# Optimization experiments

Hardware: AMD Instinct MI355X
Metric: run time of the kernel (lower is better)

## Reference

```python
import jax, jax.numpy as jnp
import numpy as np

EPS = 1e-8  # torch.nn.CosineSimilarity default eps


def _cosine_sim(a, b):
    # cosine similarity along channel dim (axis=1), matching torch semantics:
    # dot / (max(||a||, eps) * max(||b||, eps))
    na = jnp.maximum(jnp.sqrt(jnp.sum(a * a, axis=1)), EPS)
    nb = jnp.maximum(jnp.sqrt(jnp.sum(b * b, axis=1)), EPS)
    return jnp.sum(a * b, axis=1) / (na * nb)  # [B, T]


def setup_inputs() -> dict:
    key = jax.random.key(0)
    k1, k2, k3 = jax.random.split(key, 3)
    B, C, T, O, K = 8, 512, 4096, 512, 3
    feature = jax.random.normal(k1, (B, C, T), dtype=jnp.float32)
    embedding = jax.random.normal(k2, (B, C, T), dtype=jnp.float32)
    weight = jax.random.normal(k3, (O, C, K), dtype=jnp.float32) * 0.05
    return {"feature": feature, "embedding": embedding, "weight": weight}


def reference(feature, embedding, weight):
    B, C, T = feature.shape
    O = weight.shape[0]
    K = 3  # kernel_size is structurally 3 in this module

    # shifted embeddings with zero padding (left / right neighbors)
    emb_l = jnp.pad(embedding[:, :, :-1], ((0, 0), (0, 0), (1, 0)))
    emb_r = jnp.pad(embedding[:, :, 1:], ((0, 0), (0, 0), (0, 1)))
    sim = jnp.stack(
        [_cosine_sim(embedding, emb_l),
         _cosine_sim(embedding, embedding),
         _cosine_sim(embedding, emb_r)],
        axis=1,
    )  # [B, 3, T]

    # tile: first C rows = sim_l, next C = sim_c, last C = sim_r -> [B, 3C, T]
    att = jnp.repeat(sim, C, axis=1)

    # im2col (nn.Unfold with kernel (3,1), padding (1,0)): channel-major layout
    f_pad = jnp.pad(feature, ((0, 0), (0, 0), (1, 1)))  # [B, C, T+2]
    inp_unf = jnp.stack([f_pad[:, :, k:k + T] for k in range(K)], axis=2)
    inp_unf = inp_unf.reshape(B, C * K, T)  # row index = c*3 + k (torch unfold order)

    w_flat = weight.reshape(O, C * K)
    # out[b,o,t] = sum_i (inp_unf * att)[b,i,t] * w_flat[o,i]
    out = jnp.einsum('bit,oi->bot', inp_unf * att, w_flat)
    return out
```

## Files before the change

kernel.cpp:

```cpp
#include <hip/hip_runtime.h>
#include <hip/hip_bf16.h>
#include <stdint.h>

#define B_ 8
#define C_ 512
#define T_ 4096
#define O_ 512
#define KP_ 1728
#define EPS_ 1e-8f

#define BM 256
#define BN 128
#define FTP_ROWS 4104

#define RING_USH 12288
#define LDS_BYTES (4 * RING_USH * 2)

typedef unsigned short ushort_t;
typedef __attribute__((ext_vector_type(4))) float f32x4;
typedef __attribute__((ext_vector_type(8))) short bf16x8;

__device__ __forceinline__ ushort_t f2bf(float f) {
  union { float f; uint32_t u; } x; x.f = f;
  uint32_t u = x.u;
  uint32_t r = (u + 0x7FFFu + ((u >> 16) & 1u)) >> 16;
  return (ushort_t)r;
}

#define GLOAD16(gsrc, ldst) \
  __builtin_amdgcn_global_load_lds((const __attribute__((address_space(1))) unsigned int*)(gsrc), \
                                   (__attribute__((address_space(3))) unsigned int*)(ldst), 16, 0, 0)

__global__ void sim_reduce_kernel(const float* __restrict__ emb,
                                  float* __restrict__ nn_out,
                                  float* __restrict__ dl_out) {
  const int b = blockIdx.y;
  const int t0 = (blockIdx.x * 64 + threadIdx.x) * 4;
  const int cty = threadIdx.y;
  float nn0=0.f,nn1=0.f,nn2=0.f,nn3=0.f;
  float dl0=0.f,dl1=0.f,dl2=0.f,dl3=0.f;
  const float* base = emb + (size_t)b * C_ * T_;
  for (int c = cty * 128; c < cty * 128 + 128; ++c) {
    const float* row = base + (size_t)c * T_;
    float4 v = *(const float4*)(row + t0);
    float el = (t0 > 0) ? row[t0 - 1] : 0.f;
    nn0 += v.x*v.x; nn1 += v.y*v.y; nn2 += v.z*v.z; nn3 += v.w*v.w;
    dl0 += v.x*el;  dl1 += v.y*v.x; dl2 += v.z*v.y; dl3 += v.w*v.z;
  }
  __shared__ float red[4][64*8];
  float* myr = &red[cty][threadIdx.x * 8];
  if (cty != 0) {
    myr[0]=nn0; myr[1]=nn1; myr[2]=nn2; myr[3]=nn3;
    myr[4]=dl0; myr[5]=dl1; myr[6]=dl2; myr[7]=dl3;
  }
  __syncthreads();
  if (cty == 0) {
    for (int q = 1; q < 4; ++q) {
      float* r = &red[q][threadIdx.x * 8];
      nn0+=r[0]; nn1+=r[1]; nn2+=r[2]; nn3+=r[3];
      dl0+=r[4]; dl1+=r[5]; dl2+=r[6]; dl3+=r[7];
    }
    float* nb = nn_out + (size_t)b * T_ + t0;
    float* db = dl_out + (size_t)b * T_ + t0;
    nb[0]=nn0; nb[1]=nn1; nb[2]=nn2; nb[3]=nn3;
    db[0]=dl0; db[1]=dl1; db[2]=dl2; db[3]=dl3;
  }
}

__global__ void prep_small_kernel(const float* __restrict__ nn,
                                  const float* __restrict__ dl,
                                  float* __restrict__ sim,
                                  const float* __restrict__ w,
                                  ushort_t* __restrict__ wbf) {
  const int bid = blockIdx.x;
  if (bid < 128) {
    const int idx = bid * 256 + threadIdx.x;
    const int b = idx >> 12;
    const int t = idx & (T_ - 1);
    const float* nnb = nn + (size_t)b * T_;
    const float* dlb = dl + (size_t)b * T_;
    float nncur = nnb[t];
    float ncur = fmaxf(sqrtf(nncur), EPS_);
    float sc = nncur / (ncur * ncur);
    float sl = 0.f, sr = 0.f;
    if (t > 0) {
      float np = fmaxf(sqrtf(nnb[t - 1]), EPS_);
      sl = dlb[t] / (ncur * np);
    }
    if (t < T_ - 1) {
      float nx = fmaxf(sqrtf(nnb[t + 1]), EPS_);
      sr = dlb[t + 1] / (ncur * nx);
    }
    float* simb = sim + (size_t)b * 3 * T_;
    simb[t] = sl;
    simb[T_ + t] = sc;
    simb[2 * T_ + t] = sr;
  } else {
    const int idx = (bid - 128) * 256 + threadIdx.x;
    if (idx >= O_ * KP_) return;
    const int o = idx / KP_;
    const int p = idx - o * KP_;
    const int g = p / 576; const int r = p - g * 576;
    const int k = r / 192; const int j = r - k * 192;
    const int c_lo = (512 * g - k + 2) / 3;
    const int c_hi = (512 * g + 511 - k) / 3;
    const int c = (c_lo & ~7) + j;
    float v = (c >= c_lo && c <= c_hi) ? w[((size_t)o * C_ + c) * 3 + k] : 0.f;
    wbf[idx] = f2bf(v);
  }
}

__global__ void transpose_kernel(const float* __restrict__ feat, ushort_t* __restrict__ Ftp) {
  const int b = blockIdx.z;
  const int c0 = blockIdx.y * 64;
  const int tid = threadIdx.x;
  if (blockIdx.x == T_ / 64) {
    if (tid < 64)        Ftp[((size_t)b * FTP_ROWS + 0) * 512 + c0 + tid] = 0;
    else if (tid < 128)  Ftp[((size_t)b * FTP_ROWS + T_ + 1) * 512 + c0 + (tid - 64)] = 0;
    return;
  }
  const int t0 = blockIdx.x * 64;
  __shared__ ushort_t LT[64 * 72];
  {
    const int cl = tid >> 2;
    const int tq = (tid & 3) * 16;
    const float* src = feat + ((size_t)b * C_ + c0 + cl) * T_ + t0 + tq;
    for (int q = 0; q < 4; ++q) {
      float4 v = *(const float4*)(src + q * 4);
      const int t = tq + q * 4;
      LT[(t + 0) * 72 + cl] = f2bf(v.x);
      LT[(t + 1) * 72 + cl] = f2bf(v.y);
      LT[(t + 2) * 72 + cl] = f2bf(v.z);
      LT[(t + 3) * 72 + cl] = f2bf(v.w);
    }
  }
  __syncthreads();
  {
    const int tl = tid >> 2;
    const int cq = (tid & 3) * 16;
    ushort_t* dst = Ftp + ((size_t)b * FTP_ROWS + t0 + tl + 1) * 512 + c0 + cq;
    *(uint4*)(dst) = *(const uint4*)&LT[tl * 72 + cq];
    *(uint4*)(dst + 8) = *(const uint4*)&LT[tl * 72 + cq + 8];
  }
}

__global__ __launch_bounds__(512, 2)
void conv_gemm_kernel(const ushort_t* __restrict__ Ftp,
                      const ushort_t* __restrict__ wbf,
                      const float* __restrict__ sim,
                      float* __restrict__ out) {
  extern __shared__ ushort_t lds[];

  const int b = blockIdx.z;
  const int oBase = blockIdx.y * BM;
  const int tBase = blockIdx.x * BN;

  const int tid = threadIdx.x;
  const int lane = tid & 63;
  const int wid = tid >> 6;
  const int wm = wid >> 1;
  const int wn = wid & 1;
  const int llo = lane & 15, lhi = lane >> 4;

  const int rdsw = ((lhi ^ ((llo >> 1) & 3)) << 3);
  const int gch = ((lane & 3) ^ ((lane >> 3) & 3)) << 3;
  const int arow = wid * 32 + (lane >> 2);
  const int brow = wid * 16 + (lane >> 2);

  const ushort_t* ftpB = Ftp + (size_t)b * FTP_ROWS * 512;
  const float* simB = sim + (size_t)b * 3 * T_;

  float sv[3][4];
#pragma unroll
  for (int g = 0; g < 3; ++g)
#pragma unroll
    for (int n = 0; n < 4; ++n) {
      sv[g][n] = simB[g * T_ + tBase + wn * 64 + n * 16 + llo];
      asm volatile("" : "+v"(sv[g][n]));
    }
  asm volatile("s_waitcnt vmcnt(0)" ::: "memory");

  f32x4 cacc[4][4], oacc[4][4];
  const f32x4 vzero = {0.f, 0.f, 0.f, 0.f};
#pragma unroll
  for (int m = 0; m < 4; ++m)
#pragma unroll
    for (int n = 0; n < 4; ++n) { cacc[m][n] = vzero; oacc[m][n] = vzero; }

  auto STAGE = [&](int u) {
    const int s2 = u >> 1, h = u & 1;
    const int g = s2 / 9, r = s2 - g * 9, k = r / 3, jb = r - k * 3;
    const int c_st = ((512 * g - k + 2) / 3) & ~7;
    ushort_t* ring = lds + (u & 3) * RING_USH;
    const ushort_t* aS = wbf + (size_t)(oBase + arow) * KP_ + s2 * 64 + h * 32 + gch;
    GLOAD16(aS, ring + wid * 1024);
    GLOAD16(aS + (size_t)16 * KP_, ring + wid * 1024 + 512);
    const ushort_t* bS = ftpB + (size_t)(tBase + brow + k) * 512 + c_st + jb * 64 + h * 32 + gch;
    GLOAD16(bS, ring + 8192 + wid * 512);
  };

  auto PHASE = [&](int u, int vm) {
    if (vm == 6)      { asm volatile("s_waitcnt vmcnt(6)" ::: "memory"); }
    else if (vm == 3) { asm volatile("s_waitcnt vmcnt(3)" ::: "memory"); }
    else              { asm volatile("s_waitcnt vmcnt(0)" ::: "memory"); }
    __builtin_amdgcn_s_barrier();
    asm volatile("" ::: "memory");

    const ushort_t* Ah = lds + (u & 3) * RING_USH;
    const ushort_t* Bh = Ah + 8192;
    bf16x8 af[4], bfv[4];
#pragma unroll
    for (int m = 0; m < 4; ++m)
      af[m] = *(const bf16x8*)&Ah[(wm * 64 + m * 16 + llo) * 32 + rdsw];
#pragma unroll
    for (int n = 0; n < 4; ++n)
      bfv[n] = *(const bf16x8*)&Bh[(wn * 64 + n * 16 + llo) * 32 + rdsw];

    if (u + 3 < 54) STAGE(u + 3);

    __builtin_amdgcn_s_setprio(1);
#pragma unroll
    for (int m = 0; m < 4; ++m)
#pragma unroll
      for (int n = 0; n < 4; ++n)
        cacc[m][n] = __builtin_amdgcn_mfma_f32_16x16x32_bf16(af[m], bfv[n], cacc[m][n], 0, 0, 0);
    __builtin_amdgcn_s_setprio(0);

    asm volatile("s_waitcnt lgkmcnt(0)" ::: "memory");
    __builtin_amdgcn_sched_barrier(0);
  };

  STAGE(0); STAGE(1); STAGE(2);

#pragma unroll
  for (int s = 0; s < 27; ++s) {
    const int u0 = 2 * s, u1 = 2 * s + 1;
    PHASE(u0, u0 < 52 ? 6 : 3);
    PHASE(u1, u1 < 52 ? 6 : 0);
    if (s == 8 || s == 17 || s == 26) {
      const int g = s / 9;
#pragma unroll
      for (int n = 0; n < 4; ++n) {
        const float sc = sv[g][n];
#pragma unroll
        for (int m = 0; m < 4; ++m) {
          oacc[m][n] += sc * cacc[m][n];
          cacc[m][n] = vzero;
        }
      }
    }
  }

  float* outB = out + ((size_t)b * O_ + oBase) * T_ + tBase;
#pragma unroll
  for (int m = 0; m < 4; ++m) {
    const int r0 = wm * 64 + m * 16 + lhi * 4;
#pragma unroll
    for (int n = 0; n < 4; ++n) {
      const int cg = wn * 64 + n * 16 + llo;
#pragma unroll
      for (int r = 0; r < 4; ++r)
        outB[(size_t)(r0 + r) * T_ + cg] = oacc[m][n][r];
    }
  }
}

extern "C" void kernel_launch(void* const* d_in, const int* in_sizes, int n_in,
                              void* d_out, int out_size, void* d_ws, size_t ws_size,
                              hipStream_t stream) {
  const float* feature   = (const float*)d_in[0];
  const float* embedding = (const float*)d_in[1];
  const float* weight    = (const float*)d_in[2];
  float* out = (float*)d_out;

  float* ws  = (float*)d_ws;
  float* nn  = ws;
  float* dl  = nn + (size_t)B_ * T_;
  float* sim = dl + (size_t)B_ * T_;
  ushort_t* wbf = (ushort_t*)(sim + (size_t)3 * B_ * T_);
  ushort_t* Ftp = wbf + (size_t)O_ * KP_;

  (void)hipFuncSetAttribute((const void*)conv_gemm_kernel,
                            hipFuncAttributeMaxDynamicSharedMemorySize, LDS_BYTES);

  sim_reduce_kernel<<<dim3(T_ / 256, B_), dim3(64, 4), 0, stream>>>(embedding, nn, dl);
  prep_small_kernel<<<dim3(128 + (O_ * KP_ + 255) / 256), 256, 0, stream>>>(nn, dl, sim, weight, wbf);
  transpose_kernel<<<dim3(T_ / 64 + 1, C_ / 64, B_), 256, 0, stream>>>(feature, Ftp);
  conv_gemm_kernel<<<dim3(T_ / BN, O_ / BM, B_), 512, LDS_BYTES, stream>>>(Ftp, wbf, sim, out);
}
```

Measured before the change: 115.4 us.

## Load weight A-fragments directly from global into registers, stage only B in LDS

The GEMM kernel no longer stages weight tiles through LDS. Each wave loads its A fragments straight from global memory into double-buffered registers one step ahead, and only the feature (B) tiles go through a smaller 4-slot LDS ring, now static shared memory. This cuts LDS footprint and traffic and drops the A-side LDS reads and barrier dependence, with waitcnt values retuned for the changed number of in-flight loads. In exchange, A is read from global by both wn waves without coalescing-friendly staging, which raises global/L2 traffic and register pressure.

Result: slower. 177.3 us (+53.6%).

```diff
diff --git a/kernel.cpp b/kernel.cpp
--- a/kernel.cpp
+++ b/kernel.cpp
@@ -12,9 +12,6 @@
 #define BM 256
 #define BN 128
 #define FTP_ROWS 4104
-
-#define RING_USH 12288
-#define LDS_BYTES (4 * RING_USH * 2)
 
 typedef unsigned short ushort_t;
 typedef __attribute__((ext_vector_type(4))) float f32x4;
@@ -149,7 +146,7 @@
                       const ushort_t* __restrict__ wbf,
                       const float* __restrict__ sim,
                       float* __restrict__ out) {
-  extern __shared__ ushort_t lds[];
+  __shared__ __align__(16) ushort_t lds[4 * 4096];
 
   const int b = blockIdx.z;
   const int oBase = blockIdx.y * BM;
@@ -164,11 +161,14 @@
 
   const int rdsw = ((lhi ^ ((llo >> 1) & 3)) << 3);
   const int gch = ((lane & 3) ^ ((lane >> 3) & 3)) << 3;
-  const int arow = wid * 32 + (lane >> 2);
-  const int brow = wid * 16 + (lane >> 2);
 
   const ushort_t* ftpB = Ftp + (size_t)b * FTP_ROWS * 512;
   const float* simB = sim + (size_t)b * 3 * T_;
+
+  const ushort_t* aB0 = wbf + (size_t)(oBase + wm * 64 + llo) * KP_ + lhi * 8;
+  const ushort_t* aB[4] = {aB0, aB0 + 16 * KP_, aB0 + 32 * KP_, aB0 + 48 * KP_};
+
+  const ushort_t* bRow = ftpB + (size_t)(tBase + wid * 16 + (lane >> 2)) * 512 + gch;
 
   float sv[3][4];
 #pragma unroll
@@ -187,58 +187,60 @@
 #pragma unroll
     for (int n = 0; n < 4; ++n) { cacc[m][n] = vzero; oacc[m][n] = vzero; }
 
-  auto STAGE = [&](int u) {
-    const int s2 = u >> 1, h = u & 1;
+  auto GLOADB = [&](int v) {
+    const int s2 = v >> 1, h = v & 1;
     const int g = s2 / 9, r = s2 - g * 9, k = r / 3, jb = r - k * 3;
     const int c_st = ((512 * g - k + 2) / 3) & ~7;
-    ushort_t* ring = lds + (u & 3) * RING_USH;
-    const ushort_t* aS = wbf + (size_t)(oBase + arow) * KP_ + s2 * 64 + h * 32 + gch;
-    GLOAD16(aS, ring + wid * 1024);
-    GLOAD16(aS + (size_t)16 * KP_, ring + wid * 1024 + 512);
-    const ushort_t* bS = ftpB + (size_t)(tBase + brow + k) * 512 + c_st + jb * 64 + h * 32 + gch;
-    GLOAD16(bS, ring + 8192 + wid * 512);
+    GLOAD16(bRow + k * 512 + c_st + jb * 64 + h * 32, lds + (v & 3) * 4096 + wid * 512);
   };
 
-  auto PHASE = [&](int u, int vm) {
-    if (vm == 6)      { asm volatile("s_waitcnt vmcnt(6)" ::: "memory"); }
-    else if (vm == 3) { asm volatile("s_waitcnt vmcnt(3)" ::: "memory"); }
-    else              { asm volatile("s_waitcnt vmcnt(0)" ::: "memory"); }
+  bf16x8 af[2][4];
+
+  GLOADB(0); GLOADB(1); GLOADB(2);
+  __builtin_amdgcn_sched_barrier(0);
+#pragma unroll
+  for (int m = 0; m < 4; ++m)
+    af[0][m] = *(const bf16x8*)(aB[m]);
+  __builtin_amdgcn_sched_barrier(0);
+
+#pragma unroll
+  for (int u = 0; u < 54; ++u) {
+    if (u == 0)       { asm volatile("s_waitcnt vmcnt(6)"  ::: "memory"); }
+    else if (u == 1)  { asm volatile("s_waitcnt vmcnt(10)" ::: "memory"); }
+    else if (u == 52) { asm volatile("s_waitcnt vmcnt(13)" ::: "memory"); }
+    else if (u == 53) { asm volatile("s_waitcnt vmcnt(12)" ::: "memory"); }
+    else              { asm volatile("s_waitcnt vmcnt(14)" ::: "memory"); }
+    __builtin_amdgcn_sched_barrier(0);
     __builtin_amdgcn_s_barrier();
-    asm volatile("" ::: "memory");
-
-    const ushort_t* Ah = lds + (u & 3) * RING_USH;
-    const ushort_t* Bh = Ah + 8192;
-    bf16x8 af[4], bfv[4];
+    __builtin_amdgcn_sched_barrier(0);
+
+    if (u + 3 < 54) GLOADB(u + 3);
+    __builtin_amdgcn_sched_barrier(0);
+
+    if (u + 1 < 54) {
+#pragma unroll
+      for (int m = 0; m < 4; ++m)
+        af[(u + 1) & 1][m] = *(const bf16x8*)(aB[m] + (u + 1) * 32);
+    }
+    __builtin_amdgcn_sched_barrier(0);
+
+    const ushort_t* Bs = lds + (u & 3) * 4096;
+    bf16x8 bfv[4];
+#pragma unroll
+    for (int n = 0; n < 4; ++n)
+      bfv[n] = *(const bf16x8*)&Bs[(wn * 64 + n * 16 + llo) * 32 + rdsw];
+
+    __builtin_amdgcn_s_setprio(1);
 #pragma unroll
     for (int m = 0; m < 4; ++m)
-      af[m] = *(const bf16x8*)&Ah[(wm * 64 + m * 16 + llo) * 32 + rdsw];
-#pragma unroll
-    for (int n = 0; n < 4; ++n)
-      bfv[n] = *(const bf16x8*)&Bh[(wn * 64 + n * 16 + llo) * 32 + rdsw];
-
-    if (u + 3 < 54) STAGE(u + 3);
-
-    __builtin_amdgcn_s_setprio(1);
-#pragma unroll
-    for (int m = 0; m < 4; ++m)
 #pragma unroll
       for (int n = 0; n < 4; ++n)
-        cacc[m][n] = __builtin_amdgcn_mfma_f32_16x16x32_bf16(af[m], bfv[n], cacc[m][n], 0, 0, 0);
+        cacc[m][n] = __builtin_amdgcn_mfma_f32_16x16x32_bf16(af[u & 1][m], bfv[n], cacc[m][n], 0, 0, 0);
     __builtin_amdgcn_s_setprio(0);
-
-    asm volatile("s_waitcnt lgkmcnt(0)" ::: "memory");
-    __builtin_amdgcn_sched_barrier(0);
-  };
-
-  STAGE(0); STAGE(1); STAGE(2);
-
-#pragma unroll
-  for (int s = 0; s < 27; ++s) {
-    const int u0 = 2 * s, u1 = 2 * s + 1;
-    PHASE(u0, u0 < 52 ? 6 : 3);
-    PHASE(u1, u1 < 52 ? 6 : 0);
-    if (s == 8 || s == 17 || s == 26) {
-      const int g = s / 9;
+    __builtin_amdgcn_sched_barrier(0);
+
+    if (u == 17 || u == 35 || u == 53) {
+      const int g = u / 18;
 #pragma unroll
       for (int n = 0; n < 4; ++n) {
         const float sc = sv[g][n];
@@ -280,11 +282,8 @@
   ushort_t* wbf = (ushort_t*)(sim + (size_t)3 * B_ * T_);
   ushort_t* Ftp = wbf + (size_t)O_ * KP_;
 
-  (void)hipFuncSetAttribute((const void*)conv_gemm_kernel,
-                            hipFuncAttributeMaxDynamicSharedMemorySize, LDS_BYTES);
-
   sim_reduce_kernel<<<dim3(T_ / 256, B_), dim3(64, 4), 0, stream>>>(embedding, nn, dl);
   prep_small_kernel<<<dim3(128 + (O_ * KP_ + 255) / 256), 256, 0, stream>>>(nn, dl, sim, weight, wbf);
   transpose_kernel<<<dim3(T_ / 64 + 1, C_ / 64, B_), 256, 0, stream>>>(feature, Ftp);
-  conv_gemm_kernel<<<dim3(T_ / BN, O_ / BM, B_), 512, LDS_BYTES, stream>>>(Ftp, wbf, sim, out);
-}
+  conv_gemm_kernel<<<dim3(T_ / BN, O_ / BM, B_), 512, 0, stream>>>(Ftp, wbf, sim, out);
+}
```

## Widen conv GEMM tile to 256x256 and fold similarity scaling into one accumulator

Applied to the files above, without the earlier changes.

The time tile per block grows from 128 to 256 columns, and each wave now computes a 128x64 output sub-tile, so every loaded weight fragment feeds twice as many MFMAs. This raises arithmetic intensity and halves the grid. The separate output accumulator is removed: the K slabs are reordered (left, right, center), and the running accumulator is rescaled by ratios of the three similarity weights between groups, giving L*s_l + R*s_r + C*s_c in a single set of registers. The ratio trick clamps small denominators to 1e-6, which risks precision loss or wrong results when similarities are near zero. The larger LDS footprint and register pressure may also limit occupancy.

Result: faster. 112.7 us (-2.4%).

```diff
diff --git a/kernel.cpp b/kernel.cpp
--- a/kernel.cpp
+++ b/kernel.cpp
@@ -10,11 +10,11 @@
 #define EPS_ 1e-8f
 
 #define BM 256
-#define BN 128
+#define BN 256
 #define FTP_ROWS 4104
 
-#define RING_USH 12288
-#define LDS_BYTES (4 * RING_USH * 2)
+#define SLOT_USH 16384
+#define LDS_BYTES (4 * SLOT_USH * 2)
 
 typedef unsigned short ushort_t;
 typedef __attribute__((ext_vector_type(4))) float f32x4;
@@ -144,6 +144,10 @@
   }
 }
 
+__device__ __forceinline__ constexpr int slab_of_u(int u) {
+  return (u < 18) ? (u >> 1) : ((u < 36) ? (u >> 1) + 9 : (u >> 1) - 9);
+}
+
 __global__ __launch_bounds__(512, 2)
 void conv_gemm_kernel(const ushort_t* __restrict__ Ftp,
                       const ushort_t* __restrict__ wbf,
@@ -158,109 +162,112 @@
   const int tid = threadIdx.x;
   const int lane = tid & 63;
   const int wid = tid >> 6;
-  const int wm = wid >> 1;
-  const int wn = wid & 1;
+  const int wm = wid >> 2;
+  const int wn = wid & 3;
   const int llo = lane & 15, lhi = lane >> 4;
 
   const int rdsw = ((lhi ^ ((llo >> 1) & 3)) << 3);
   const int gch = ((lane & 3) ^ ((lane >> 3) & 3)) << 3;
-  const int arow = wid * 32 + (lane >> 2);
-  const int brow = wid * 16 + (lane >> 2);
+  const int srow = wid * 32 + (lane >> 2);
 
   const ushort_t* ftpB = Ftp + (size_t)b * FTP_ROWS * 512;
   const float* simB = sim + (size_t)b * 3 * T_;
 
-  float sv[3][4];
-#pragma unroll
-  for (int g = 0; g < 3; ++g)
-#pragma unroll
-    for (int n = 0; n < 4; ++n) {
-      sv[g][n] = simB[g * T_ + tBase + wn * 64 + n * 16 + llo];
-      asm volatile("" : "+v"(sv[g][n]));
-    }
+  const ushort_t* aSrc = wbf + (size_t)(oBase + srow) * KP_ + gch;
+  const ushort_t* bRow = ftpB + (size_t)(tBase + srow) * 512 + gch;
+
+  float rat0[4], rat1[4], fin[4];
+#pragma unroll
+  for (int n = 0; n < 4; ++n) {
+    const int col = tBase + wn * 64 + n * 16 + llo;
+    float s_l = simB[col];
+    float s_c = simB[T_ + col];
+    float s_r = simB[2 * T_ + col];
+    float shr = (fabsf(s_r) < 1e-6f) ? copysignf(1e-6f, s_r) : s_r;
+    float shc = fmaxf(s_c, 1e-6f);
+    rat0[n] = s_l / shr;
+    rat1[n] = shr / shc;
+    fin[n]  = s_c;
+    asm volatile("" : "+v"(rat0[n]), "+v"(rat1[n]), "+v"(fin[n]));
+  }
   asm volatile("s_waitcnt vmcnt(0)" ::: "memory");
 
-  f32x4 cacc[4][4], oacc[4][4];
+  f32x4 cacc[8][4];
   const f32x4 vzero = {0.f, 0.f, 0.f, 0.f};
 #pragma unroll
-  for (int m = 0; m < 4; ++m)
-#pragma unroll
-    for (int n = 0; n < 4; ++n) { cacc[m][n] = vzero; oacc[m][n] = vzero; }
+  for (int m = 0; m < 8; ++m)
+#pragma unroll
+    for (int n = 0; n < 4; ++n) cacc[m][n] = vzero;
 
   auto STAGE = [&](int u) {
-    const int s2 = u >> 1, h = u & 1;
+    const int s2 = slab_of_u(u), h = u & 1;
     const int g = s2 / 9, r = s2 - g * 9, k = r / 3, jb = r - k * 3;
     const int c_st = ((512 * g - k + 2) / 3) & ~7;
-    ushort_t* ring = lds + (u & 3) * RING_USH;
-    const ushort_t* aS = wbf + (size_t)(oBase + arow) * KP_ + s2 * 64 + h * 32 + gch;
-    GLOAD16(aS, ring + wid * 1024);
-    GLOAD16(aS + (size_t)16 * KP_, ring + wid * 1024 + 512);
-    const ushort_t* bS = ftpB + (size_t)(tBase + brow + k) * 512 + c_st + jb * 64 + h * 32 + gch;
-    GLOAD16(bS, ring + 8192 + wid * 512);
+    ushort_t* slot = lds + (u & 3) * SLOT_USH;
+    const ushort_t* aS = aSrc + s2 * 64 + h * 32;
+    GLOAD16(aS, slot + wid * 1024);
+    GLOAD16(aS + (size_t)16 * KP_, slot + wid * 1024 + 512);
+    const ushort_t* bS = bRow + k * 512 + c_st + jb * 64 + h * 32;
+    GLOAD16(bS, slot + 8192 + wid * 1024);
+    GLOAD16(bS + (size_t)16 * 512, slot + 8192 + wid * 1024 + 512);
   };
 
-  auto PHASE = [&](int u, int vm) {
-    if (vm == 6)      { asm volatile("s_waitcnt vmcnt(6)" ::: "memory"); }
-    else if (vm == 3) { asm volatile("s_waitcnt vmcnt(3)" ::: "memory"); }
+  STAGE(0); STAGE(1); STAGE(2);
+  __builtin_amdgcn_sched_barrier(0);
+
+#pragma unroll
+  for (int u = 0; u < 54; ++u) {
+    if (u <= 51)      { asm volatile("s_waitcnt vmcnt(8)" ::: "memory"); }
+    else if (u == 52) { asm volatile("s_waitcnt vmcnt(4)" ::: "memory"); }
     else              { asm volatile("s_waitcnt vmcnt(0)" ::: "memory"); }
+    __builtin_amdgcn_sched_barrier(0);
     __builtin_amdgcn_s_barrier();
-    asm volatile("" ::: "memory");
-
-    const ushort_t* Ah = lds + (u & 3) * RING_USH;
+    __builtin_amdgcn_sched_barrier(0);
+
+    if (u + 3 < 54) STAGE(u + 3);
+    __builtin_amdgcn_sched_barrier(0);
+
+    const ushort_t* Ah = lds + (u & 3) * SLOT_USH;
     const ushort_t* Bh = Ah + 8192;
-    bf16x8 af[4], bfv[4];
-#pragma unroll
-    for (int m = 0; m < 4; ++m)
-      af[m] = *(const bf16x8*)&Ah[(wm * 64 + m * 16 + llo) * 32 + rdsw];
+    bf16x8 af[8], bfv[4];
+#pragma unroll
+    for (int m = 0; m < 8; ++m)
+      af[m] = *(const bf16x8*)&Ah[(wm * 128 + m * 16 + llo) * 32 + rdsw];
 #pragma unroll
     for (int n = 0; n < 4; ++n)
       bfv[n] = *(const bf16x8*)&Bh[(wn * 64 + n * 16 + llo) * 32 + rdsw];
 
-    if (u + 3 < 54) STAGE(u + 3);
-
     __builtin_amdgcn_s_setprio(1);
 #pragma unroll
-    for (int m = 0; m < 4; ++m)
+    for (int m = 0; m < 8; ++m)
 #pragma unroll
       for (int n = 0; n < 4; ++n)
         cacc[m][n] = __builtin_amdgcn_mfma_f32_16x16x32_bf16(af[m], bfv[n], cacc[m][n], 0, 0, 0);
     __builtin_amdgcn_s_setprio(0);
 
+    if (u == 17 || u == 35 || u == 53) {
+#pragma unroll
+      for (int n = 0; n < 4; ++n) {
+        const float sc = (u == 17) ? rat0[n] : (u == 35) ? rat1[n] : fin[n];
+#pragma unroll
+        for (int m = 0; m < 8; ++m) cacc[m][n] *= sc;
+      }
+    }
+
     asm volatile("s_waitcnt lgkmcnt(0)" ::: "memory");
     __builtin_amdgcn_sched_barrier(0);
-  };
-
-  STAGE(0); STAGE(1); STAGE(2);
-
-#pragma unroll
-  for (int s = 0; s < 27; ++s) {
-    const int u0 = 2 * s, u1 = 2 * s + 1;
-    PHASE(u0, u0 < 52 ? 6 : 3);
-    PHASE(u1, u1 < 52 ? 6 : 0);
-    if (s == 8 || s == 17 || s == 26) {
-      const int g = s / 9;
-#pragma unroll
-      for (int n = 0; n < 4; ++n) {
-        const float sc = sv[g][n];
-#pragma unroll
-        for (int m = 0; m < 4; ++m) {
-          oacc[m][n] += sc * cacc[m][n];
-          cacc[m][n] = vzero;
-        }
-      }
-    }
   }
 
   float* outB = out + ((size_t)b * O_ + oBase) * T_ + tBase;
 #pragma unroll
-  for (int m = 0; m < 4; ++m) {
-    const int r0 = wm * 64 + m * 16 + lhi * 4;
+  for (int m = 0; m < 8; ++m) {
+    const int r0 = wm * 128 + m * 16 + lhi * 4;
 #pragma unroll
     for (int n = 0; n < 4; ++n) {
       const int cg = wn * 64 + n * 16 + llo;
 #pragma unroll
       for (int r = 0; r < 4; ++r)
-        outB[(size_t)(r0 + r) * T_ + cg] = oacc[m][n][r];
+        outB[(size_t)(r0 + r) * T_ + cg] = cacc[m][n][r];
     }
   }
 }
```
